# Kernel tuning notes

Hardware: AMD Instinct MI355X
Metric: run time of the kernel (lower is better)

## Reference

```python
import jax, jax.numpy as jnp
import numpy as np

KERNEL_SIZE = 3  # stations.kernel_size
IMAGE_W = 1.0    # loss.weights.image
STATION_W = 0.5  # loss.weights.station


def setup_inputs() -> dict:
    key = jax.random.key(0)
    k1, k2, k3, k4 = jax.random.split(key, 4)
    B, H, W = 32, 1024, 1024
    S = 256
    return {
        "predictions": jax.random.normal(k1, (B, 1, H, W), dtype=jnp.float32),
        "targets": jax.random.normal(k2, (B, 1, H // 2, W // 2), dtype=jnp.float32),
        "station_positions": jax.random.randint(k3, (B, S, 2), 0, H, dtype=jnp.int32),
        "station_runoffs": jax.random.normal(k4, (B, S), dtype=jnp.float32),
    }


def _combined_loss(predictions, targets, station_positions, station_runoffs):
    B, _, H, W = predictions.shape
    # ---- ImageLoss: bilinear upsample targets (align_corners=False == half-pixel) then MSE
    if targets.shape != predictions.shape:
        targets = jax.image.resize(targets, predictions.shape, method="bilinear")
    img_loss = jnp.mean((predictions - targets) ** 2)

    # ---- StationLoss: clipped kxk box mean at each station, MSE vs runoff
    kh = KERNEL_SIZE // 2
    offs = jnp.arange(-kh, kh + 1)                     # (K,)
    px = station_positions[..., 0]                     # (B,S) x coord -> width axis
    py = station_positions[..., 1]                     # (B,S) y coord -> height axis
    ys = py[..., None] + offs                          # (B,S,K)
    xs = px[..., None] + offs                          # (B,S,K)
    vy = (ys >= 0) & (ys < H)
    vx = (xs >= 0) & (xs < W)
    ysc = jnp.clip(ys, 0, H - 1)
    xsc = jnp.clip(xs, 0, W - 1)
    pred2d = predictions[:, 0]                         # (B,H,W)
    bidx = jnp.arange(B)[:, None, None, None]
    vals = pred2d[bidx, ysc[:, :, :, None], xsc[:, :, None, :]]   # (B,S,K,K)
    mask = (vy[:, :, :, None] & vx[:, :, None, :]).astype(predictions.dtype)
    count = jnp.sum(mask, axis=(-2, -1))               # (B,S) always >= 1 (center in-bounds)
    box_mean = jnp.sum(vals * mask, axis=(-2, -1)) / count
    stn_loss = jnp.mean((box_mean - station_runoffs) ** 2)

    total = IMAGE_W * img_loss + STATION_W * stn_loss
    return total, img_loss, stn_loss


def reference(predictions, targets, station_positions, station_runoffs):
    return _combined_loss(predictions, targets, station_positions, station_runoffs)
```

## Files before the change

kernel.cpp:

```cpp
#include <hip/hip_runtime.h>
#include <stdint.h>

#define BATCH 32
#define HDIM  1024
#define WDIM  1024
#define H2    (HDIM / 2)
#define W2    (WDIM / 2)
#define NSTN  256

__device__ __forceinline__ float blockReduceSum(float v) {
    #pragma unroll
    for (int off = 32; off > 0; off >>= 1)
        v += __shfl_down(v, off, 64);
    __shared__ float smem[16];
    const int lane = threadIdx.x & 63;
    const int wid  = threadIdx.x >> 6;
    if (lane == 0) smem[wid] = v;
    __syncthreads();
    const int nw = (blockDim.x + 63) >> 6;
    v = (threadIdx.x < nw) ? smem[threadIdx.x] : 0.0f;
    if (wid == 0) {
        #pragma unroll
        for (int off = 8; off > 0; off >>= 1)
            v += __shfl_down(v, off, 64);
    }
    return v;
}

__global__ void img_loss_kernel(const float* __restrict__ pred,
                                const float* __restrict__ tgt,
                                float* __restrict__ acc) {
    const int64_t total4 = (int64_t)BATCH * HDIM * (WDIM / 4);
    float lsum = 0.0f;
    for (int64_t i = (int64_t)blockIdx.x * blockDim.x + threadIdx.x; i < total4;
         i += (int64_t)gridDim.x * blockDim.x) {
        const int x4   = (int)(i % (WDIM / 4));
        const int64_t rest = i / (WDIM / 4);
        const int y = (int)(rest % HDIM);
        const int b = (int)(rest / HDIM);
        const int x0 = x4 * 4;

        const float4 p = *(const float4*)(pred + ((int64_t)b * HDIM + y) * WDIM + x0);

        const int my = y >> 1;
        int yA, yB; float wyA, wyB;
        if ((y & 1) == 0) { yA = (my - 1 < 0) ? 0 : my - 1; yB = my; wyA = 0.25f; wyB = 0.75f; }
        else              { yA = my; yB = (my + 1 >= H2) ? H2 - 1 : my + 1; wyA = 0.75f; wyB = 0.25f; }

        const float* tA = tgt + ((int64_t)b * H2 + yA) * W2;
        const float* tB = tgt + ((int64_t)b * H2 + yB) * W2;

        const int m0  = x0 >> 1;
        const int xm1 = (m0 - 1 < 0) ? 0 : m0 - 1;
        const int xp2 = (m0 + 2 >= W2) ? W2 - 1 : m0 + 2;

        const float r0 = wyA * tA[xm1]    + wyB * tB[xm1];
        const float r1 = wyA * tA[m0]     + wyB * tB[m0];
        const float r2 = wyA * tA[m0 + 1] + wyB * tB[m0 + 1];
        const float r3 = wyA * tA[xp2]    + wyB * tB[xp2];

        const float t0 = 0.25f * r0 + 0.75f * r1;
        const float t1 = 0.75f * r1 + 0.25f * r2;
        const float t2 = 0.25f * r1 + 0.75f * r2;
        const float t3 = 0.75f * r2 + 0.25f * r3;

        const float d0 = p.x - t0, d1 = p.y - t1, d2 = p.z - t2, d3 = p.w - t3;
        lsum += d0 * d0 + d1 * d1 + d2 * d2 + d3 * d3;
    }
    const float bs = blockReduceSum(lsum);
    if (threadIdx.x == 0) atomicAdd(acc, bs);
}

__global__ void stn_loss_kernel(const float* __restrict__ pred,
                                const int* __restrict__ pos,
                                const float* __restrict__ runoff,
                                float* __restrict__ acc) {
    const int idx = blockIdx.x * blockDim.x + threadIdx.x;
    float lsum = 0.0f;
    if (idx < BATCH * NSTN) {
        const int b = idx / NSTN;
        const int px = pos[idx * 2 + 0];
        const int py = pos[idx * 2 + 1];
        const float* p = pred + (int64_t)b * HDIM * WDIM;
        float sum = 0.0f; int cnt = 0;
        #pragma unroll
        for (int dy = -1; dy <= 1; ++dy) {
            const int y = py + dy;
            if (y < 0 || y >= HDIM) continue;
            #pragma unroll
            for (int dx = -1; dx <= 1; ++dx) {
                const int x = px + dx;
                if (x < 0 || x >= WDIM) continue;
                sum += p[(int64_t)y * WDIM + x];
                cnt++;
            }
        }
        const float d = sum / (float)cnt - runoff[idx];
        lsum = d * d;
    }
    const float bs = blockReduceSum(lsum);
    if (threadIdx.x == 0) atomicAdd(acc, bs);
}

__global__ void finalize_kernel(const float* __restrict__ acc,
                                float* __restrict__ out) {
    const float img = acc[0] * (1.0f / ((float)BATCH * HDIM * WDIM));
    const float stn = acc[1] * (1.0f / ((float)BATCH * NSTN));
    out[0] = img + 0.5f * stn;
    out[1] = img;
    out[2] = stn;
}

extern "C" void kernel_launch(void* const* d_in, const int* in_sizes, int n_in,
                              void* d_out, int out_size, void* d_ws, size_t ws_size,
                              hipStream_t stream) {
    const float* pred   = (const float*)d_in[0];
    const float* tgt    = (const float*)d_in[1];
    const int*   pos    = (const int*)d_in[2];
    const float* runoff = (const float*)d_in[3];
    float* out = (float*)d_out;
    float* acc = (float*)d_ws;

    hipMemsetAsync(acc, 0, 2 * sizeof(float), stream);

    img_loss_kernel<<<2048, 256, 0, stream>>>(pred, tgt, acc);

    stn_loss_kernel<<<(BATCH * NSTN + 255) / 256, 256, 0, stream>>>(pred, pos, runoff, acc + 1);

    finalize_kernel<<<1, 1, 0, stream>>>(acc, out);
}
```

Measured before the change: 229.5 us.

## Fuse image, station and finalize passes into one kernel with last-block reduction

Merges the image loss, station loss and finalize kernels into a single launch. The last block to finish, found through an atomic counter, writes the final outputs. Each thread now handles an even/odd output row pair, so the three target rows are loaded once and reused for both rows, and index math uses shifts instead of 64-bit div/mod. This removes two kernel launches and redundant target loads, at the cost of an extra atomic and fences per block.

```diff
diff --git a/kernel.cpp b/kernel.cpp
--- a/kernel.cpp
+++ b/kernel.cpp
@@ -7,78 +7,38 @@
 #define H2    (HDIM / 2)
 #define W2    (WDIM / 2)
 #define NSTN  256
+#define NBLOCKS 2048
+#define NTHREADS (NBLOCKS * 256)
 
-__device__ __forceinline__ float blockReduceSum(float v) {
+__device__ __forceinline__ float blockReduceSum(float v, float* smem) {
     #pragma unroll
     for (int off = 32; off > 0; off >>= 1)
         v += __shfl_down(v, off, 64);
-    __shared__ float smem[16];
     const int lane = threadIdx.x & 63;
     const int wid  = threadIdx.x >> 6;
     if (lane == 0) smem[wid] = v;
     __syncthreads();
-    const int nw = (blockDim.x + 63) >> 6;
-    v = (threadIdx.x < nw) ? smem[threadIdx.x] : 0.0f;
+    v = (threadIdx.x < 4) ? smem[threadIdx.x] : 0.0f;
     if (wid == 0) {
-        #pragma unroll
-        for (int off = 8; off > 0; off >>= 1)
-            v += __shfl_down(v, off, 64);
+        v += __shfl_down(v, 2, 64);
+        v += __shfl_down(v, 1, 64);
     }
     return v;
 }
 
-__global__ void img_loss_kernel(const float* __restrict__ pred,
-                                const float* __restrict__ tgt,
-                                float* __restrict__ acc) {
-    const int64_t total4 = (int64_t)BATCH * HDIM * (WDIM / 4);
-    float lsum = 0.0f;
-    for (int64_t i = (int64_t)blockIdx.x * blockDim.x + threadIdx.x; i < total4;
-         i += (int64_t)gridDim.x * blockDim.x) {
-        const int x4   = (int)(i % (WDIM / 4));
-        const int64_t rest = i / (WDIM / 4);
-        const int y = (int)(rest % HDIM);
-        const int b = (int)(rest / HDIM);
-        const int x0 = x4 * 4;
+__global__ __launch_bounds__(256) void fused_loss_kernel(
+        const float* __restrict__ pred,
+        const float* __restrict__ tgt,
+        const int*   __restrict__ pos,
+        const float* __restrict__ runoff,
+        float* __restrict__ acc,
+        float* __restrict__ out) {
+    __shared__ float smem[4];
 
-        const float4 p = *(const float4*)(pred + ((int64_t)b * HDIM + y) * WDIM + x0);
-
-        const int my = y >> 1;
-        int yA, yB; float wyA, wyB;
-        if ((y & 1) == 0) { yA = (my - 1 < 0) ? 0 : my - 1; yB = my; wyA = 0.25f; wyB = 0.75f; }
-        else              { yA = my; yB = (my + 1 >= H2) ? H2 - 1 : my + 1; wyA = 0.75f; wyB = 0.25f; }
-
-        const float* tA = tgt + ((int64_t)b * H2 + yA) * W2;
-        const float* tB = tgt + ((int64_t)b * H2 + yB) * W2;
-
-        const int m0  = x0 >> 1;
-        const int xm1 = (m0 - 1 < 0) ? 0 : m0 - 1;
-        const int xp2 = (m0 + 2 >= W2) ? W2 - 1 : m0 + 2;
-
-        const float r0 = wyA * tA[xm1]    + wyB * tB[xm1];
-        const float r1 = wyA * tA[m0]     + wyB * tB[m0];
-        const float r2 = wyA * tA[m0 + 1] + wyB * tB[m0 + 1];
-        const float r3 = wyA * tA[xp2]    + wyB * tB[xp2];
-
-        const float t0 = 0.25f * r0 + 0.75f * r1;
-        const float t1 = 0.75f * r1 + 0.25f * r2;
-        const float t2 = 0.25f * r1 + 0.75f * r2;
-        const float t3 = 0.75f * r2 + 0.25f * r3;
-
-        const float d0 = p.x - t0, d1 = p.y - t1, d2 = p.z - t2, d3 = p.w - t3;
-        lsum += d0 * d0 + d1 * d1 + d2 * d2 + d3 * d3;
-    }
-    const float bs = blockReduceSum(lsum);
-    if (threadIdx.x == 0) atomicAdd(acc, bs);
-}
-
-__global__ void stn_loss_kernel(const float* __restrict__ pred,
-                                const int* __restrict__ pos,
-                                const float* __restrict__ runoff,
-                                float* __restrict__ acc) {
-    const int idx = blockIdx.x * blockDim.x + threadIdx.x;
-    float lsum = 0.0f;
-    if (idx < BATCH * NSTN) {
-        const int b = idx / NSTN;
+    float stn_local = 0.0f;
+    if (blockIdx.x < 32) {
+        const int idx = blockIdx.x * 256 + threadIdx.x;
+        const int b  = idx >> 8;
         const int px = pos[idx * 2 + 0];
         const int py = pos[idx * 2 + 1];
         const float* p = pred + (int64_t)b * HDIM * WDIM;
@@ -91,24 +51,84 @@
             for (int dx = -1; dx <= 1; ++dx) {
                 const int x = px + dx;
                 if (x < 0 || x >= WDIM) continue;
-                sum += p[(int64_t)y * WDIM + x];
+                sum += p[y * WDIM + x];
                 cnt++;
             }
         }
         const float d = sum / (float)cnt - runoff[idx];
-        lsum = d * d;
+        stn_local = d * d;
     }
-    const float bs = blockReduceSum(lsum);
-    if (threadIdx.x == 0) atomicAdd(acc, bs);
-}
 
-__global__ void finalize_kernel(const float* __restrict__ acc,
-                                float* __restrict__ out) {
-    const float img = acc[0] * (1.0f / ((float)BATCH * HDIM * WDIM));
-    const float stn = acc[1] * (1.0f / ((float)BATCH * NSTN));
-    out[0] = img + 0.5f * stn;
-    out[1] = img;
-    out[2] = stn;
+    float img_local = 0.0f;
+    const int total_units = BATCH * (HDIM / 2) * (WDIM / 4);
+    for (int u = blockIdx.x * 256 + threadIdx.x; u < total_units; u += NTHREADS) {
+        const int xg = u & 255;
+        const int yp = (u >> 8) & 511;
+        const int b  = u >> 17;
+        const int x0 = xg << 2;
+        const int m0 = xg << 1;
+
+        const float* prow = pred + (((int64_t)b * HDIM + (yp << 1)) << 10) + x0;
+        const float4 pe = *(const float4*)(prow);
+        const float4 po = *(const float4*)(prow + WDIM);
+
+        const int ym1 = (yp == 0)      ? 0      : yp - 1;
+        const int yp1 = (yp == H2 - 1) ? H2 - 1 : yp + 1;
+        const int xm1 = (m0 == 0)      ? 0      : m0 - 1;
+        const int xp2 = (m0 + 2 >= W2) ? W2 - 1 : m0 + 2;
+
+        const float* tm1 = tgt + (((int64_t)b * H2 + ym1) << 9);
+        const float* t0  = tgt + (((int64_t)b * H2 + yp ) << 9);
+        const float* tp1 = tgt + (((int64_t)b * H2 + yp1) << 9);
+
+        const float am1 = tm1[xm1], a0 = tm1[m0], a1 = tm1[m0 + 1], a2 = tm1[xp2];
+        const float bm1 = t0 [xm1], b0 = t0 [m0], b1 = t0 [m0 + 1], b2 = t0 [xp2];
+        const float cm1 = tp1[xm1], c0 = tp1[m0], c1 = tp1[m0 + 1], c2 = tp1[xp2];
+
+        const float e_m1 = 0.25f * am1 + 0.75f * bm1;
+        const float e_0  = 0.25f * a0  + 0.75f * b0;
+        const float e_1  = 0.25f * a1  + 0.75f * b1;
+        const float e_2  = 0.25f * a2  + 0.75f * b2;
+        const float o_m1 = 0.75f * bm1 + 0.25f * cm1;
+        const float o_0  = 0.75f * b0  + 0.25f * c0;
+        const float o_1  = 0.75f * b1  + 0.25f * c1;
+        const float o_2  = 0.75f * b2  + 0.25f * c2;
+
+        float d0 = pe.x - (0.25f * e_m1 + 0.75f * e_0);
+        float d1 = pe.y - (0.75f * e_0  + 0.25f * e_1);
+        float d2 = pe.z - (0.25f * e_0  + 0.75f * e_1);
+        float d3 = pe.w - (0.75f * e_1  + 0.25f * e_2);
+        img_local += d0 * d0 + d1 * d1 + d2 * d2 + d3 * d3;
+
+        d0 = po.x - (0.25f * o_m1 + 0.75f * o_0);
+        d1 = po.y - (0.75f * o_0  + 0.25f * o_1);
+        d2 = po.z - (0.25f * o_0  + 0.75f * o_1);
+        d3 = po.w - (0.75f * o_1  + 0.25f * o_2);
+        img_local += d0 * d0 + d1 * d1 + d2 * d2 + d3 * d3;
+    }
+
+    const float bi = blockReduceSum(img_local, smem);
+    if (threadIdx.x == 0) atomicAdd(&acc[0], bi);
+    if (blockIdx.x < 32) {
+        __syncthreads();
+        const float bs = blockReduceSum(stn_local, smem);
+        if (threadIdx.x == 0) atomicAdd(&acc[1], bs);
+    }
+
+    if (threadIdx.x == 0) {
+        __threadfence();
+        const unsigned old = atomicAdd((unsigned*)&acc[2], 1u);
+        if (old == NBLOCKS - 1) {
+            __threadfence();
+            const float is = atomicAdd(&acc[0], 0.0f);
+            const float ss = atomicAdd(&acc[1], 0.0f);
+            const float img = is * (1.0f / ((float)BATCH * HDIM * WDIM));
+            const float stn = ss * (1.0f / ((float)BATCH * NSTN));
+            out[0] = img + 0.5f * stn;
+            out[1] = img;
+            out[2] = stn;
+        }
+    }
 }
 
 extern "C" void kernel_launch(void* const* d_in, const int* in_sizes, int n_in,
@@ -121,11 +141,6 @@
     float* out = (float*)d_out;
     float* acc = (float*)d_ws;
 
-    hipMemsetAsync(acc, 0, 2 * sizeof(float), stream);
-
-    img_loss_kernel<<<2048, 256, 0, stream>>>(pred, tgt, acc);
-
-    stn_loss_kernel<<<(BATCH * NSTN + 255) / 256, 256, 0, stream>>>(pred, pos, runoff, acc + 1);
-
-    finalize_kernel<<<1, 1, 0, stream>>>(acc, out);
+    hipMemsetAsync(acc, 0, 3 * sizeof(float), stream);
+    fused_loss_kernel<<<NBLOCKS, 256, 0, stream>>>(pred, tgt, pos, runoff, acc, out);
 }
```

New measurement: 319.2 us. 1.39x slower.
